# Optimization experiments

Measured on AMD Instinct MI355X. Metric: run time of the kernel, lower is better.

The kernel has to match this reference:

```python
import jax, jax.numpy as jnp
import numpy as np

N_HEAD = 12

def setup_inputs() -> dict:
    key = jax.random.key(0)
    ks = jax.random.split(key, 5)
    B, T, C = 8, 1024, 768
    s = 0.02
    return {
        'x': jax.random.normal(ks[0], (B, T, C), dtype=jnp.float32),
        'w_attn': jax.random.normal(ks[1], (C, 3 * C), dtype=jnp.float32) * s,
        'b_attn': jax.random.normal(ks[2], (3 * C,), dtype=jnp.float32) * s,
        'w_proj': jax.random.normal(ks[3], (C, C), dtype=jnp.float32) * s,
        'b_proj': jax.random.normal(ks[4], (C,), dtype=jnp.float32) * s,
    }

def reference(x, w_attn, b_attn, w_proj, b_proj):
    B, T, C = x.shape
    H, D = N_HEAD, C // N_HEAD
    qkv = x @ w_attn + b_attn                      # [B,T,3C]
    q, k, v = jnp.split(qkv, 3, axis=-1)
    q = q.reshape(B, T, H, D)
    k = k.reshape(B, T, H, D)
    v = v.reshape(B, T, H, D)
    # NOTE: faithful to source - NO 1/sqrt(D) scaling
    wei = jnp.einsum('bthd,bshd->bhts', q, k)      # [B,H,T,T]
    causal = jnp.tril(jnp.ones((T, T), dtype=bool))
    wei = jnp.where(causal[None, None], wei, -jnp.inf)
    wei = jax.nn.softmax(wei, axis=-1)
    out = jnp.einsum('bhts,bshd->bthd', wei, v)    # [B,T,H,D]
    out = out.reshape(B, T, C)
    return out @ w_proj + b_proj
```

## Files before the change

kernel.cpp:

```cpp
#include <hip/hip_runtime.h>

typedef __attribute__((ext_vector_type(8))) short bf16x8_t;
typedef __attribute__((ext_vector_type(4))) float f32x4_t;

#define AS1C(p) ((const __attribute__((address_space(1))) void*)(p))
#define AS3(p)  ((__attribute__((address_space(3))) void*)(p))

#define N_HEAD 12
#define SEQ_T 1024
#define CDIM 768
#define HDIM 64
#define L2E 1.44269504f

__device__ __forceinline__ unsigned short f2bf(float f) {
    union { float f; unsigned int u; } v;
    v.f = f;
    unsigned int r = (v.u + 0x7fffu + ((v.u >> 16) & 1u)) >> 16;
    return (unsigned short)r;
}

__global__ __launch_bounds__(256) void prep(
    const float4* __restrict__ x4, ushort4* __restrict__ xbf4,
    const float* __restrict__ w_attn, unsigned short* __restrict__ waT,
    const float* __restrict__ w_proj, unsigned short* __restrict__ wpT)
{
    __shared__ float tile[32][33];
    const int blk = blockIdx.x;
    const int tid = threadIdx.x;
    if (blk < 6144) {
        int i = blk * 256 + tid;
        float4 v = x4[i];
        ushort4 o;
        o.x = f2bf(v.x); o.y = f2bf(v.y); o.z = f2bf(v.z); o.w = f2bf(v.w);
        xbf4[i] = o;
        return;
    }
    const float* src; unsigned short* dst; int R, Cc, c0, r0;
    if (blk < 7872) {
        int idx = blk - 6144;
        src = w_attn; dst = waT; R = 768; Cc = 2304;
        c0 = (idx % 72) * 32; r0 = (idx / 72) * 32;
    } else {
        int idx = blk - 7872;
        src = w_proj; dst = wpT; R = 768; Cc = 768;
        c0 = (idx % 24) * 32; r0 = (idx / 24) * 32;
    }
    const int tx = tid & 31, ty = tid >> 5;
#pragma unroll
    for (int i = 0; i < 4; i++)
        tile[ty + i * 8][tx] = src[(size_t)(r0 + ty + i * 8) * Cc + c0 + tx];
    __syncthreads();
#pragma unroll
    for (int i = 0; i < 4; i++)
        dst[(size_t)(c0 + ty + i * 8) * R + r0 + tx] = f2bf(tile[tx][ty + i * 8]);
}

__device__ __forceinline__ void gemm128_core(
    const unsigned short* __restrict__ A, const unsigned short* __restrict__ Bt,
    unsigned short* As, unsigned short* Bs, f32x4_t acc[4][4], int mBase, int nBase)
{
    const int tid  = threadIdx.x;
    const int lane = tid & 63;
    const int wv   = tid >> 6;
    const int quad = lane >> 4;
    const int l16  = lane & 15;
    const int wm   = (wv >> 1) * 64;
    const int wn   = (wv & 1) * 64;

    f32x4_t zero = {0.f, 0.f, 0.f, 0.f};
#pragma unroll
    for (int tm = 0; tm < 4; tm++)
#pragma unroll
        for (int tn = 0; tn < 4; tn++)
            acc[tm][tn] = zero;

    for (int kt = 0; kt < 768; kt += 64) {
#pragma unroll
        for (int i = 0; i < 4; i++) {
            int cbase = i * 256 + wv * 64;
            int ci = cbase + lane;
            int r = ci >> 3;
            int koff = (((ci & 7) ^ (r & 7)) << 3);
            __builtin_amdgcn_global_load_lds(
                AS1C(A + (size_t)(mBase + r) * 768 + kt + koff),
                AS3(As + cbase * 8), 16, 0, 0);
            __builtin_amdgcn_global_load_lds(
                AS1C(Bt + (size_t)(nBase + r) * 768 + kt + koff),
                AS3(Bs + cbase * 8), 16, 0, 0);
        }
        __syncthreads();
#pragma unroll
        for (int ks = 0; ks < 2; ks++) {
            bf16x8_t af[4], bfv[4];
#pragma unroll
            for (int tm = 0; tm < 4; tm++)
                af[tm] = *(const bf16x8_t*)(As + (wm + tm * 16 + l16) * 64 +
                                            (((ks * 4 + quad) ^ (l16 & 7)) << 3));
#pragma unroll
            for (int tn = 0; tn < 4; tn++)
                bfv[tn] = *(const bf16x8_t*)(Bs + (wn + tn * 16 + l16) * 64 +
                                             (((ks * 4 + quad) ^ (l16 & 7)) << 3));
#pragma unroll
            for (int tm = 0; tm < 4; tm++)
#pragma unroll
                for (int tn = 0; tn < 4; tn++)
                    acc[tm][tn] = __builtin_amdgcn_mfma_f32_16x16x32_bf16(
                        af[tm], bfv[tn], acc[tm][tn], 0, 0, 0);
        }
        __syncthreads();
    }
}

__global__ __launch_bounds__(256) void gemm_qkv(
    const unsigned short* __restrict__ x, const unsigned short* __restrict__ waT,
    const float* __restrict__ b_attn,
    unsigned short* __restrict__ qbuf, unsigned short* __restrict__ kbuf,
    unsigned short* __restrict__ vbuf)
{
    __shared__ __align__(16) unsigned short As[128 * 64];
    __shared__ __align__(16) unsigned short Bs[128 * 64];
    f32x4_t acc[4][4];
    const int lid = blockIdx.x;
    const int xcd = lid & 7;
    const int j = lid >> 3;
    const int mTile = xcd * 8 + (j & 7);
    const int nTile = j >> 3;
    const int mBase = mTile * 128;
    const int nBase = nTile * 128;
    gemm128_core(x, waT, As, Bs, acc, mBase, nBase);

    const int tid = threadIdx.x;
    const int lane = tid & 63, wv = tid >> 6;
    const int quad = lane >> 4, l16 = lane & 15;
    const int wm = (wv >> 1) * 64, wn = (wv & 1) * 64;
    const int part = nTile / 6;

#pragma unroll
    for (int tn = 0; tn < 4; tn++) {
        int n = nBase + wn + tn * 16 + l16;
        float bv = b_attn[n];
        int f = n - part * 768;
        int hh = f >> 6, d = f & 63;
        if (part == 2) {
#pragma unroll
            for (int tm = 0; tm < 4; tm++) {
                int t0 = mBase + wm + tm * 16 + quad * 4;
                int bb = t0 >> 10, tt = t0 & 1023;
                ushort4 pk;
                pk.x = f2bf(acc[tm][tn][0] + bv);
                pk.y = f2bf(acc[tm][tn][1] + bv);
                pk.z = f2bf(acc[tm][tn][2] + bv);
                pk.w = f2bf(acc[tm][tn][3] + bv);
                *(ushort4*)(vbuf + ((size_t)(bb * N_HEAD + hh) * HDIM + d) * SEQ_T + tt) = pk;
            }
        } else {
            const float scale = (part == 0) ? L2E : 1.f;
            unsigned short* dst = (part == 0) ? qbuf : kbuf;
#pragma unroll
            for (int tm = 0; tm < 4; tm++) {
#pragma unroll
                for (int i = 0; i < 4; i++) {
                    int row = mBase + wm + tm * 16 + quad * 4 + i;
                    int bb = row >> 10, tt = row & 1023;
                    dst[((size_t)(bb * N_HEAD + hh) * SEQ_T + tt) * HDIM + d] =
                        f2bf((acc[tm][tn][i] + bv) * scale);
                }
            }
        }
    }
}

__device__ __forceinline__ void attn_pv(
    f32x4_t s[4], int diag, int qloc, int quad, int l16,
    float& lsum, unsigned short* pw, const bf16x8_t vf[4][2], f32x4_t o[4])
{
    if (diag) {
#pragma unroll
        for (int c = 0; c < 4; c++)
#pragma unroll
            for (int i = 0; i < 4; i++)
                if (c * 16 + quad * 4 + i > qloc) s[c][i] = -1e30f;
    }
    float p[4][4];
#pragma unroll
    for (int c = 0; c < 4; c++)
#pragma unroll
        for (int i = 0; i < 4; i++)
            p[c][i] = exp2f(s[c][i]);
#pragma unroll
    for (int c = 0; c < 4; c++)
        lsum += (p[c][0] + p[c][1]) + (p[c][2] + p[c][3]);

    unsigned int u[4][2];
#pragma unroll
    for (int c = 0; c < 4; c++)
#pragma unroll
        for (int i2 = 0; i2 < 2; i2++)
            u[c][i2] = (unsigned int)f2bf(p[c][2 * i2]) |
                       ((unsigned int)f2bf(p[c][2 * i2 + 1]) << 16);

    __asm__ __volatile__("" ::: "memory");
#pragma unroll
    for (int c = 0; c < 4; c++)
#pragma unroll
        for (int i2 = 0; i2 < 2; i2++) {
            int g = c * 2 + (quad >> 1);
            *(unsigned int*)(pw + l16 * 64 + ((g ^ (l16 & 7)) << 3) +
                             4 * (quad & 1) + 2 * i2) = u[c][i2];
        }
    __asm__ __volatile__("" ::: "memory");
    bf16x8_t pf[2];
#pragma unroll
    for (int kc = 0; kc < 2; kc++)
        pf[kc] = *(const bf16x8_t*)(pw + l16 * 64 + (((kc * 4 + quad) ^ (l16 & 7)) << 3));
    __asm__ __volatile__("" ::: "memory");
#pragma unroll
    for (int kc = 0; kc < 2; kc++)
#pragma unroll
        for (int nc = 0; nc < 4; nc++)
            o[nc] = __builtin_amdgcn_mfma_f32_16x16x32_bf16(pf[kc], vf[nc][kc], o[nc], 0, 0, 0);
}

__global__ __launch_bounds__(256, 3) void attn_fused(
    const unsigned short* __restrict__ qb, const unsigned short* __restrict__ kb,
    const unsigned short* __restrict__ vb, unsigned short* __restrict__ attb)
{
    __shared__ __align__(16) unsigned short Kbuf[2][64 * 64];
    __shared__ __align__(16) unsigned short Vbuf[2][64 * 64];
    __shared__ __align__(16) unsigned short Psh[4][16 * 64];

    const int bhx = blockIdx.x;
    const int t   = blockIdx.y;
    const int h = bhx % N_HEAD;
    const int b = bhx / N_HEAD;
    const int tid = threadIdx.x;
    const int lane = tid & 63, wv = tid >> 6;
    const int quad = lane >> 4, l16 = lane & 15;
    const int tB = 15 - t, kmax = 15 - t;
    const int qloc = wv * 16 + l16;

    const size_t bh = (size_t)(b * N_HEAD + h);
    const unsigned short* kbase = kb + bh * SEQ_T * HDIM;
    const unsigned short* vbase = vb + bh * HDIM * SEQ_T;
    const unsigned short* qpt   = qb + bh * SEQ_T * HDIM;

    const int j0 = wv * 128 + lane, j1 = j0 + 64;
    const int r0 = j0 >> 3, g0 = (j0 & 7) ^ (r0 & 7);
    const int r1 = j1 >> 3, g1 = (j1 & 7) ^ (r1 & 7);
    const int rgK0 = r0 * 64 + g0 * 8,   rgK1 = r1 * 64 + g1 * 8;
    const int rgV0 = r0 * 1024 + g0 * 8, rgV1 = r1 * 1024 + g1 * 8;
    const int ldsc0 = (wv * 128) * 8, ldsc1 = (wv * 128 + 64) * 8;

    bf16x8_t qfA[2], qfB[2];
    {
        const unsigned short* qa  = qpt + (size_t)(t * 64 + qloc) * HDIM;
        const unsigned short* qbp = qpt + (size_t)(tB * 64 + qloc) * HDIM;
#pragma unroll
        for (int kc = 0; kc < 2; kc++) {
            qfA[kc] = *(const bf16x8_t*)(qa + kc * 32 + quad * 8);
            qfB[kc] = *(const bf16x8_t*)(qbp + kc * 32 + quad * 8);
        }
    }

    f32x4_t zero = {0.f, 0.f, 0.f, 0.f};
    f32x4_t oA[4], oB[4];
#pragma unroll
    for (int c = 0; c < 4; c++) { oA[c] = zero; oB[c] = zero; }
    float lA = 0.f, lB = 0.f;

    __builtin_amdgcn_global_load_lds(AS1C(kbase + rgK0), AS3(&Kbuf[0][0] + ldsc0), 16, 0, 0);
    __builtin_amdgcn_global_load_lds(AS1C(kbase + rgK1), AS3(&Kbuf[0][0] + ldsc1), 16, 0, 0);
    __builtin_amdgcn_global_load_lds(AS1C(vbase + rgV0), AS3(&Vbuf[0][0] + ldsc0), 16, 0, 0);
    __builtin_amdgcn_global_load_lds(AS1C(vbase + rgV1), AS3(&Vbuf[0][0] + ldsc1), 16, 0, 0);
    __syncthreads();

    for (int kt = 0; kt <= kmax; kt++) {
        const int cur = kt & 1, nxt = cur ^ 1;
        if (kt < kmax) {
            const unsigned short* kp = kbase + (kt + 1) * 4096;
            const unsigned short* vp = vbase + (kt + 1) * 64;
            __builtin_amdgcn_global_load_lds(AS1C(kp + rgK0), AS3(&Kbuf[nxt][0] + ldsc0), 16, 0, 0);
            __builtin_amdgcn_global_load_lds(AS1C(kp + rgK1), AS3(&Kbuf[nxt][0] + ldsc1), 16, 0, 0);
            __builtin_amdgcn_global_load_lds(AS1C(vp + rgV0), AS3(&Vbuf[nxt][0] + ldsc0), 16, 0, 0);
            __builtin_amdgcn_global_load_lds(AS1C(vp + rgV1), AS3(&Vbuf[nxt][0] + ldsc1), 16, 0, 0);
        }

        const unsigned short* Kc = &Kbuf[cur][0];
        const unsigned short* Vc = &Vbuf[cur][0];
        const int doA = (kt <= t);

        bf16x8_t vf[4][2];
#pragma unroll
        for (int nc = 0; nc < 4; nc++)
#pragma unroll
            for (int kc = 0; kc < 2; kc++)
                vf[nc][kc] = *(const bf16x8_t*)(Vc + (nc * 16 + l16) * 64 +
                                                (((kc * 4 + quad) ^ (l16 & 7)) << 3));

        f32x4_t sB[4], sA[4];
#pragma unroll
        for (int c = 0; c < 4; c++) {
            bf16x8_t kf0 = *(const bf16x8_t*)(Kc + (c * 16 + l16) * 64 +
                                              ((quad ^ (l16 & 7)) << 3));
            bf16x8_t kf1 = *(const bf16x8_t*)(Kc + (c * 16 + l16) * 64 +
                                              (((4 + quad) ^ (l16 & 7)) << 3));
            sB[c] = __builtin_amdgcn_mfma_f32_16x16x32_bf16(kf0, qfB[0], zero, 0, 0, 0);
            sB[c] = __builtin_amdgcn_mfma_f32_16x16x32_bf16(kf1, qfB[1], sB[c], 0, 0, 0);
            if (doA) {
                sA[c] = __builtin_amdgcn_mfma_f32_16x16x32_bf16(kf0, qfA[0], zero, 0, 0, 0);
                sA[c] = __builtin_amdgcn_mfma_f32_16x16x32_bf16(kf1, qfA[1], sA[c], 0, 0, 0);
            }
        }

        unsigned short* pw = &Psh[wv][0];
        attn_pv(sB, kt == tB, qloc, quad, l16, lB, pw, vf, oB);
        if (doA)
            attn_pv(sA, kt == t, qloc, quad, l16, lA, pw, vf, oA);
        __syncthreads();
    }

    lA += __shfl_xor(lA, 16); lA += __shfl_xor(lA, 32);
    lB += __shfl_xor(lB, 16); lB += __shfl_xor(lB, 32);
    float invA = 1.f / lA, invB = 1.f / lB;
    float iA[4], iB[4];
#pragma unroll
    for (int i = 0; i < 4; i++) {
        iA[i] = __shfl(invA, quad * 4 + i);
        iB[i] = __shfl(invB, quad * 4 + i);
    }

#pragma unroll
    for (int nc = 0; nc < 4; nc++)
#pragma unroll
        for (int i = 0; i < 4; i++) {
            int rowA = t * 64 + wv * 16 + quad * 4 + i;
            int rowB = tB * 64 + wv * 16 + quad * 4 + i;
            int col = h * HDIM + nc * 16 + l16;
            attb[((size_t)b * SEQ_T + rowA) * CDIM + col] = f2bf(oA[nc][i] * iA[i]);
            attb[((size_t)b * SEQ_T + rowB) * CDIM + col] = f2bf(oB[nc][i] * iB[i]);
        }
}

__global__ __launch_bounds__(256) void gemm_proj(
    const unsigned short* __restrict__ attb, const unsigned short* __restrict__ wpT,
    const float* __restrict__ b_proj, float* __restrict__ out)
{
    __shared__ __align__(16) unsigned short As[128 * 64];
    __shared__ __align__(16) unsigned short Bs[128 * 64];
    f32x4_t acc[4][4];
    const int lid = blockIdx.x;
    const int xcd = lid & 7;
    const int j = lid >> 3;
    const int mTile = xcd * 8 + (j & 7);
    const int nTile = j >> 3;
    const int mBase = mTile * 128;
    const int nBase = nTile * 128;
    gemm128_core(attb, wpT, As, Bs, acc, mBase, nBase);

    const int tid = threadIdx.x;
    const int lane = tid & 63, wv = tid >> 6;
    const int quad = lane >> 4, l16 = lane & 15;
    const int wm = (wv >> 1) * 64, wn = (wv & 1) * 64;

#pragma unroll
    for (int tn = 0; tn < 4; tn++) {
        int n = nBase + wn + tn * 16 + l16;
        float bv = b_proj[n];
#pragma unroll
        for (int tm = 0; tm < 4; tm++)
#pragma unroll
            for (int i = 0; i < 4; i++) {
                int row = mBase + wm + tm * 16 + quad * 4 + i;
                out[(size_t)row * CDIM + n] = acc[tm][tn][i] + bv;
            }
    }
}

extern "C" void kernel_launch(void* const* d_in, const int* in_sizes, int n_in,
                              void* d_out, int out_size, void* d_ws, size_t ws_size,
                              hipStream_t stream) {
    const float* x      = (const float*)d_in[0];
    const float* w_attn = (const float*)d_in[1];
    const float* b_attn = (const float*)d_in[2];
    const float* w_proj = (const float*)d_in[3];
    const float* b_proj = (const float*)d_in[4];
    float* out = (float*)d_out;

    unsigned short* ws   = (unsigned short*)d_ws;
    unsigned short* waT  = ws;
    unsigned short* wpT  = waT + 1769472;
    unsigned short* xbf  = wpT + 589824;
    unsigned short* qbuf = xbf + 6291456;
    unsigned short* kbuf = qbuf + 6291456;
    unsigned short* vbuf = kbuf + 6291456;
    unsigned short* attb = vbuf + 6291456;

    prep<<<dim3(8448), 256, 0, stream>>>((const float4*)x, (ushort4*)xbf,
                                         w_attn, waT, w_proj, wpT);
    gemm_qkv<<<dim3(1152), 256, 0, stream>>>(xbf, waT, b_attn, qbuf, kbuf, vbuf);
    attn_fused<<<dim3(96, 8), 256, 0, stream>>>(qbuf, kbuf, vbuf, attb);
    gemm_proj<<<dim3(384), 256, 0, stream>>>(attb, wpT, b_proj, out);
}
```

Before: 188.6 us.

## Interleave dual-tile softmax with PV MFMAs and use 64x128 proj GEMM tiles

The attention loop now computes the exp/pack for both query tiles before running either PV matmul, so the second tile's softmax work can overlap the first tile's MFMA chain instead of running strictly after it. The output projection GEMM switches from 128x128 to 64x128 tiles with its own inline loop, doubling the grid to 768 blocks so more CUs have work. The smaller tile lowers reuse per block and loses any prefetching that gemm128_core may have had, since the new loop loads and then synchronises each k-step with no double buffering.

```diff
diff --git a/kernel.cpp b/kernel.cpp
--- a/kernel.cpp
+++ b/kernel.cpp
@@ -170,9 +170,9 @@
     }
 }
 
-__device__ __forceinline__ void attn_pv(
-    f32x4_t s[4], int diag, int qloc, int quad, int l16,
-    float& lsum, unsigned short* pw, const bf16x8_t vf[4][2], f32x4_t o[4])
+__device__ __forceinline__ void mask_exp_pack(
+    f32x4_t s[4], int diag, int qloc, int quad,
+    float& lsum, unsigned int u[4][2])
 {
     if (diag) {
 #pragma unroll
@@ -190,16 +190,17 @@
 #pragma unroll
     for (int c = 0; c < 4; c++)
         lsum += (p[c][0] + p[c][1]) + (p[c][2] + p[c][3]);
-
-    unsigned int u[4][2];
 #pragma unroll
     for (int c = 0; c < 4; c++)
 #pragma unroll
         for (int i2 = 0; i2 < 2; i2++)
             u[c][i2] = (unsigned int)f2bf(p[c][2 * i2]) |
                        ((unsigned int)f2bf(p[c][2 * i2 + 1]) << 16);
-
-    __asm__ __volatile__("" ::: "memory");
+}
+
+__device__ __forceinline__ void p_write(
+    unsigned short* pw, const unsigned int u[4][2], int quad, int l16)
+{
 #pragma unroll
     for (int c = 0; c < 4; c++)
 #pragma unroll
@@ -208,17 +209,6 @@
             *(unsigned int*)(pw + l16 * 64 + ((g ^ (l16 & 7)) << 3) +
                              4 * (quad & 1) + 2 * i2) = u[c][i2];
         }
-    __asm__ __volatile__("" ::: "memory");
-    bf16x8_t pf[2];
-#pragma unroll
-    for (int kc = 0; kc < 2; kc++)
-        pf[kc] = *(const bf16x8_t*)(pw + l16 * 64 + (((kc * 4 + quad) ^ (l16 & 7)) << 3));
-    __asm__ __volatile__("" ::: "memory");
-#pragma unroll
-    for (int kc = 0; kc < 2; kc++)
-#pragma unroll
-        for (int nc = 0; nc < 4; nc++)
-            o[nc] = __builtin_amdgcn_mfma_f32_16x16x32_bf16(pf[kc], vf[nc][kc], o[nc], 0, 0, 0);
 }
 
 __global__ __launch_bounds__(256, 3) void attn_fused(
@@ -313,9 +303,37 @@
         }
 
         unsigned short* pw = &Psh[wv][0];
-        attn_pv(sB, kt == tB, qloc, quad, l16, lB, pw, vf, oB);
+        unsigned int uB[4][2], uA[4][2];
+
+        mask_exp_pack(sB, kt == tB, qloc, quad, lB, uB);
+        __asm__ __volatile__("" ::: "memory");
+        p_write(pw, uB, quad, l16);
         if (doA)
-            attn_pv(sA, kt == t, qloc, quad, l16, lA, pw, vf, oA);
+            mask_exp_pack(sA, kt == t, qloc, quad, lA, uA);
+        __asm__ __volatile__("" ::: "memory");
+        bf16x8_t pfB[2];
+#pragma unroll
+        for (int kc = 0; kc < 2; kc++)
+            pfB[kc] = *(const bf16x8_t*)(pw + l16 * 64 + (((kc * 4 + quad) ^ (l16 & 7)) << 3));
+        __asm__ __volatile__("" ::: "memory");
+#pragma unroll
+        for (int kc = 0; kc < 2; kc++)
+#pragma unroll
+            for (int nc = 0; nc < 4; nc++)
+                oB[nc] = __builtin_amdgcn_mfma_f32_16x16x32_bf16(pfB[kc], vf[nc][kc], oB[nc], 0, 0, 0);
+        if (doA) {
+            p_write(pw, uA, quad, l16);
+            __asm__ __volatile__("" ::: "memory");
+            bf16x8_t pfA[2];
+#pragma unroll
+            for (int kc = 0; kc < 2; kc++)
+                pfA[kc] = *(const bf16x8_t*)(pw + l16 * 64 + (((kc * 4 + quad) ^ (l16 & 7)) << 3));
+#pragma unroll
+            for (int kc = 0; kc < 2; kc++)
+#pragma unroll
+                for (int nc = 0; nc < 4; nc++)
+                    oA[nc] = __builtin_amdgcn_mfma_f32_16x16x32_bf16(pfA[kc], vf[nc][kc], oA[nc], 0, 0, 0);
+        }
         __syncthreads();
     }
 
@@ -345,29 +363,81 @@
     const unsigned short* __restrict__ attb, const unsigned short* __restrict__ wpT,
     const float* __restrict__ b_proj, float* __restrict__ out)
 {
-    __shared__ __align__(16) unsigned short As[128 * 64];
+    __shared__ __align__(16) unsigned short As[64 * 64];
     __shared__ __align__(16) unsigned short Bs[128 * 64];
-    f32x4_t acc[4][4];
     const int lid = blockIdx.x;
     const int xcd = lid & 7;
     const int j = lid >> 3;
-    const int mTile = xcd * 8 + (j & 7);
-    const int nTile = j >> 3;
-    const int mBase = mTile * 128;
+    const int mTile = xcd * 16 + (j & 15);
+    const int nTile = j >> 4;
+    const int mBase = mTile * 64;
     const int nBase = nTile * 128;
-    gemm128_core(attb, wpT, As, Bs, acc, mBase, nBase);
-
-    const int tid = threadIdx.x;
-    const int lane = tid & 63, wv = tid >> 6;
-    const int quad = lane >> 4, l16 = lane & 15;
-    const int wm = (wv >> 1) * 64, wn = (wv & 1) * 64;
+
+    const int tid  = threadIdx.x;
+    const int lane = tid & 63;
+    const int wv   = tid >> 6;
+    const int quad = lane >> 4;
+    const int l16  = lane & 15;
+    const int wm   = (wv >> 1) * 32;
+    const int wn   = (wv & 1) * 64;
+
+    f32x4_t zero = {0.f, 0.f, 0.f, 0.f};
+    f32x4_t acc[2][4];
+#pragma unroll
+    for (int tm = 0; tm < 2; tm++)
+#pragma unroll
+        for (int tn = 0; tn < 4; tn++)
+            acc[tm][tn] = zero;
+
+    for (int kt = 0; kt < 768; kt += 64) {
+#pragma unroll
+        for (int i = 0; i < 2; i++) {
+            int cbase = i * 256 + wv * 64;
+            int ci = cbase + lane;
+            int r = ci >> 3;
+            int koff = (((ci & 7) ^ (r & 7)) << 3);
+            __builtin_amdgcn_global_load_lds(
+                AS1C(attb + (size_t)(mBase + r) * 768 + kt + koff),
+                AS3(As + cbase * 8), 16, 0, 0);
+        }
+#pragma unroll
+        for (int i = 0; i < 4; i++) {
+            int cbase = i * 256 + wv * 64;
+            int ci = cbase + lane;
+            int r = ci >> 3;
+            int koff = (((ci & 7) ^ (r & 7)) << 3);
+            __builtin_amdgcn_global_load_lds(
+                AS1C(wpT + (size_t)(nBase + r) * 768 + kt + koff),
+                AS3(Bs + cbase * 8), 16, 0, 0);
+        }
+        __syncthreads();
+#pragma unroll
+        for (int ks = 0; ks < 2; ks++) {
+            bf16x8_t af[2], bfv[4];
+#pragma unroll
+            for (int tm = 0; tm < 2; tm++)
+                af[tm] = *(const bf16x8_t*)(As + (wm + tm * 16 + l16) * 64 +
+                                            (((ks * 4 + quad) ^ (l16 & 7)) << 3));
+#pragma unroll
+            for (int tn = 0; tn < 4; tn++)
+                bfv[tn] = *(const bf16x8_t*)(Bs + (wn + tn * 16 + l16) * 64 +
+                                             (((ks * 4 + quad) ^ (l16 & 7)) << 3));
+#pragma unroll
+            for (int tm = 0; tm < 2; tm++)
+#pragma unroll
+                for (int tn = 0; tn < 4; tn++)
+                    acc[tm][tn] = __builtin_amdgcn_mfma_f32_16x16x32_bf16(
+                        af[tm], bfv[tn], acc[tm][tn], 0, 0, 0);
+        }
+        __syncthreads();
+    }
 
 #pragma unroll
     for (int tn = 0; tn < 4; tn++) {
         int n = nBase + wn + tn * 16 + l16;
         float bv = b_proj[n];
 #pragma unroll
-        for (int tm = 0; tm < 4; tm++)
+        for (int tm = 0; tm < 2; tm++)
 #pragma unroll
             for (int i = 0; i < 4; i++) {
                 int row = mBase + wm + tm * 16 + quad * 4 + i;
@@ -399,5 +469,5 @@
                                          w_attn, waT, w_proj, wpT);
     gemm_qkv<<<dim3(1152), 256, 0, stream>>>(xbf, waT, b_attn, qbuf, kbuf, vbuf);
     attn_fused<<<dim3(96, 8), 256, 0, stream>>>(qbuf, kbuf, vbuf, attb);
-    gemm_proj<<<dim3(384), 256, 0, stream>>>(attb, wpT, b_proj, out);
-}
+    gemm_proj<<<dim3(768), 256, 0, stream>>>(attb, wpT, b_proj, out);
+}
```

Result: no change. 187.5 us (-0.6%).
